# Kernel optimization log

Hardware: AMD Instinct MI355X
Metric: run time of the kernel (lower is better)

The kernel has to match this reference:

```python
import jax, jax.numpy as jnp
import numpy as np

B, F, R, L, P = 16384, 64, 1024, 4, 128  # batch, features, rules, max conditions, interaction pairs


def setup_inputs() -> dict:
    key = jax.random.key(0)
    ks = jax.random.split(key, 8)
    x = jax.random.normal(ks[0], (B, F), dtype=jnp.float32)
    attention_weights = jax.random.uniform(ks[1], (F,), dtype=jnp.float32, minval=0.5, maxval=1.5)
    premise_params = jnp.ones((R,), dtype=jnp.float32)
    rule_threshs = jax.random.normal(ks[2], (R, L), dtype=jnp.float32)
    # signs are +/-1 (split direction of each XGBoost condition)
    rule_signs = jnp.where(jax.random.randint(ks[3], (R, L), 0, 2) == 1, 1.0, -1.0).astype(jnp.float32)
    rule_masks = (jax.random.uniform(ks[4], (R, L)) < 0.9).astype(jnp.float32)
    rule_masks = rule_masks.at[:, 0].set(1.0)
    consequent_params = jax.random.normal(ks[5], (R, 1 + F + F + P), dtype=jnp.float32) * 0.01
    rule_feat_idxs = jax.random.randint(ks[6], (R, L), 0, F)
    interaction_pairs = jax.random.randint(ks[7], (P, 2), 0, F)
    return {
        "x": x,
        "attention_weights": attention_weights,
        "premise_params": premise_params,
        "rule_threshs": rule_threshs,
        "rule_signs": rule_signs,
        "rule_masks": rule_masks,
        "consequent_params": consequent_params,
        "rule_feat_idxs": rule_feat_idxs,
        "interaction_pairs": interaction_pairs,
    }


def reference(x, attention_weights, premise_params, rule_threshs, rule_signs,
              rule_masks, consequent_params, rule_feat_idxs, interaction_pairs):
    # attention scaling
    x_att = x * attention_weights  # [B, F]

    # --- fuzzify_and_infer ---
    sel = x_att[:, rule_feat_idxs]  # gather -> [B, R, L]
    z = premise_params[None, :, None] * (sel - rule_threshs[None]) * rule_signs[None]
    mf = jax.nn.sigmoid(z)
    masked_mf = mf * rule_masks[None] + (1.0 - rule_masks[None])  # inactive conds -> 1
    firing = jnp.prod(masked_mf, axis=2)  # [B, R]
    w = firing / (jnp.sum(firing, axis=1, keepdims=True) + 1e-8)  # normalized firing

    # --- TSK polynomials (order=2 with interactions): [x, x^2, xi*xj, 1] ---
    inter = x_att[:, interaction_pairs[:, 0]] * x_att[:, interaction_pairs[:, 1]]  # [B, P]
    ones = jnp.ones((x.shape[0], 1), dtype=x.dtype)
    p = jnp.concatenate([x_att, x_att * x_att, inter, ones], axis=1)  # [B, 1+2F+P]

    # weighted consequent sum: y_b = sum_r w_br * (p_b . theta_r)
    y = jnp.einsum('br,bi,ri->b', w, p, consequent_params)
    return y
```

## Files before the change

### kernel.cpp

```cpp
#include <hip/hip_runtime.h>

typedef short short8 __attribute__((ext_vector_type(8)));
typedef float f32x4 __attribute__((ext_vector_type(4)));


#define OFF_CP   0ULL
#define OFF_CB   524288ULL
#define OFF_A2   528384ULL
#define OFF_C2   544768ULL
#define OFF_IX   561152ULL
#define OFF_PAIR 565248ULL
#define OFF_NUM  565504ULL
#define OFF_DEN  631040ULL

#define XS 65

__device__ __forceinline__ unsigned short f2bf(float f) {
  unsigned u = __float_as_uint(f);
  return (unsigned short)((u + 0x7FFFu + ((u >> 16) & 1u)) >> 16);
}

__global__ __launch_bounds__(256) void prep_kernel(
    const float* __restrict__ pp, const float* __restrict__ th,
    const float* __restrict__ sg, const float* __restrict__ mk,
    const float* __restrict__ cp, const int* __restrict__ fidx,
    const int* __restrict__ pairs, unsigned char* __restrict__ ws)
{
  unsigned short* cp_out = (unsigned short*)(ws + OFF_CP);
  float* cbo = (float*)(ws + OFF_CB);
  float* a2o = (float*)(ws + OFF_A2);
  float* c2o = (float*)(ws + OFF_C2);
  unsigned* ixo = (unsigned*)(ws + OFF_IX);
  unsigned short* pro = (unsigned short*)(ws + OFF_PAIR);
  int bid = blockIdx.x, t = threadIdx.x;

  if (bid < 256) {
    int e = bid * 1024 + t * 4;
    int r = e >> 8, c = e & 255;
    const float* src = cp + (size_t)r * 257 + c;
#pragma unroll
    for (int q = 0; q < 4; ++q) cp_out[e + q] = f2bf(src[q]);
  } else if (bid < 260) {
    int r = (bid - 256) * 256 + t;
    float p = pp[r];
    unsigned pk = 0;
#pragma unroll
    for (int l = 0; l < 4; ++l) {
      float m = mk[r * 4 + l], s = sg[r * 4 + l], tt = th[r * 4 + l];
      float A, C;
      if (m != 0.f) { A = -1.44269504f * p * s; C = 1.44269504f * p * s * tt; }
      else          { A = 0.f;                  C = -126.f; }
      a2o[r * 4 + l] = A; c2o[r * 4 + l] = C;
      pk |= ((unsigned)fidx[r * 4 + l] & 0xFFu) << (8 * l);
    }
    ixo[r] = pk;
    cbo[r] = cp[(size_t)r * 257 + 256];
  } else if (bid == 260) {
    if (t < 128)
      pro[t] = (unsigned short)((pairs[2 * t] & 0xFF) | ((pairs[2 * t + 1] & 0xFF) << 8));
  } else {
    float* dst = (float*)(ws + (bid == 261 ? OFF_NUM : OFF_DEN));
#pragma unroll
    for (int q = 0; q < 64; ++q) dst[q * 256 + t] = 0.f;
  }
}

__global__ __launch_bounds__(256, 3) void main_kernel(
    const unsigned char* __restrict__ ws,
    const float* __restrict__ x, const float* __restrict__ att,
    float* __restrict__ numg, float* __restrict__ deng)
{
  __shared__ float xa[64 * XS];
  __shared__ short lCP[256 * 32];
  __shared__ short lP[64 * 32];
  __shared__ unsigned short lPair[128];

  const unsigned short* CP = (const unsigned short*)(ws + OFF_CP);
  const float* CB = (const float*)(ws + OFF_CB);
  const float4* A2p = (const float4*)(ws + OFF_A2);
  const float4* C2p = (const float4*)(ws + OFF_C2);
  const unsigned* IX = (const unsigned*)(ws + OFF_IX);
  const unsigned short* PRW = (const unsigned short*)(ws + OFF_PAIR);

  int t = threadIdx.x, l = t & 63, w = t >> 6;
  int g = l >> 4, lr = l & 15;
  int b0 = blockIdx.x * 64, r0 = blockIdx.y * 256;

  if (t < 128) lPair[t] = PRW[t];
  {
#pragma unroll
    for (int i = 0; i < 4; ++i) {
      int idx = t + i * 256, row = idx >> 4, c4 = idx & 15;
      float4 a4 = ((const float4*)att)[c4];
      float4 v = ((const float4*)(x + (size_t)(b0 + row) * 64))[c4];
      float* dst = &xa[row * XS + c4 * 4];
      dst[0] = v.x * a4.x; dst[1] = v.y * a4.y;
      dst[2] = v.z * a4.z; dst[3] = v.w * a4.w;
    }
  }
  __syncthreads();

  f32x4 acc[4][4];
#pragma unroll
  for (int mi = 0; mi < 4; ++mi)
#pragma unroll
    for (int ni = 0; ni < 4; ++ni)
      acc[mi][ni] = (f32x4){0.f, 0.f, 0.f, 0.f};

  int row2 = t >> 2, q = t & 3;
  int sw2 = (row2 ^ (row2 >> 2)) & 3;
  const float* xr2 = &xa[row2 * XS];
  const unsigned short* cpbase = CP + (size_t)(r0 + row2) * 256 + q * 8;

  short8 cpr[2][4];
#pragma unroll
  for (int i = 0; i < 4; ++i) {
    cpr[0][i] = *(const short8*)(cpbase + (size_t)i * 64 * 256);
    cpr[1][i] = *(const short8*)(cpbase + (size_t)i * 64 * 256 + 32);
  }

#pragma unroll 2
  for (int ks = 0; ks < 8; ++ks) {
    int k0 = ks * 32;
    int fb = k0 + q * 8;
    short8 vp;
    if (ks < 2) {
#pragma unroll
      for (int j = 0; j < 8; ++j) vp[j] = f2bf(xr2[fb + j]);
    } else if (ks < 4) {
#pragma unroll
      for (int j = 0; j < 8; ++j) { float u = xr2[fb - 64 + j]; vp[j] = f2bf(u * u); }
    } else {
      const unsigned* pw = (const unsigned*)&lPair[fb - 128];
#pragma unroll
      for (int u = 0; u < 4; ++u) {
        unsigned pk = pw[u];
        vp[2 * u]     = f2bf(xr2[pk & 255] * xr2[(pk >> 8) & 255]);
        vp[2 * u + 1] = f2bf(xr2[(pk >> 16) & 255] * xr2[pk >> 24]);
      }
    }
    __syncthreads();
#pragma unroll
    for (int i = 0; i < 4; ++i) {
      int rowc = row2 + i * 64;
      int swc = (rowc ^ (rowc >> 2)) & 3;
      *(short8*)&lCP[rowc * 32 + ((q ^ swc) * 8)] = cpr[ks & 1][i];
    }
    *(short8*)&lP[row2 * 32 + ((q ^ sw2) * 8)] = vp;
    if (ks < 6) {
#pragma unroll
      for (int i = 0; i < 4; ++i)
        cpr[ks & 1][i] = *(const short8*)(cpbase + (size_t)i * 64 * 256 + k0 + 64);
    }
    __syncthreads();
    short8 bF[4];
#pragma unroll
    for (int ni = 0; ni < 4; ++ni) {
      int row = ni * 16 + lr;
      int s = (row ^ (row >> 2)) & 3;
      bF[ni] = *(const short8*)&lP[row * 32 + ((g ^ s) * 8)];
    }
#pragma unroll
    for (int mi = 0; mi < 4; ++mi) {
      int row = w * 64 + mi * 16 + lr;
      int s = (row ^ (row >> 2)) & 3;
      short8 aF = *(const short8*)&lCP[row * 32 + ((g ^ s) * 8)];
#pragma unroll
      for (int ni = 0; ni < 4; ++ni)
        acc[mi][ni] = __builtin_amdgcn_mfma_f32_16x16x32_bf16(aF, bF[ni], acc[mi][ni], 0, 0, 0);
    }
  }

  float num[4] = {0.f, 0.f, 0.f, 0.f}, den[4] = {0.f, 0.f, 0.f, 0.f};
#pragma unroll
  for (int mi = 0; mi < 4; ++mi) {
#pragma unroll
    for (int j = 0; j < 4; ++j) {
      int rule = r0 + w * 64 + mi * 16 + (g << 2) + j;
      float4 A2 = A2p[rule], C2 = C2p[rule];
      unsigned pk = IX[rule];
      float bias = CB[rule];
      int f0 = pk & 255, f1 = (pk >> 8) & 255, f2 = (pk >> 16) & 255, f3 = pk >> 24;
#pragma unroll
      for (int ni = 0; ni < 4; ++ni) {
        const float* xr = &xa[(ni * 16 + lr) * XS];
        float D = 1.f;
        float e0 = exp2f(fmaf(A2.x, xr[f0], C2.x)); D = fmaf(D, e0, D);
        float e1 = exp2f(fmaf(A2.y, xr[f1], C2.y)); D = fmaf(D, e1, D);
        float e2 = exp2f(fmaf(A2.z, xr[f2], C2.z)); D = fmaf(D, e2, D);
        float e3 = exp2f(fmaf(A2.w, xr[f3], C2.w)); D = fmaf(D, e3, D);
        float fir = __builtin_amdgcn_rcpf(D);
        num[ni] = fmaf(fir, acc[mi][ni][j] + bias, num[ni]);
        den[ni] += fir;
      }
    }
  }

#pragma unroll
  for (int ni = 0; ni < 4; ++ni) {
    float n = num[ni], d = den[ni];
    n += __shfl_xor(n, 16, 64); n += __shfl_xor(n, 32, 64);
    d += __shfl_xor(d, 16, 64); d += __shfl_xor(d, 32, 64);
    num[ni] = n; den[ni] = d;
  }
  float nv = 0.f, dv = 0.f;
#pragma unroll
  for (int ni = 0; ni < 4; ++ni)
    if (g == ni) { nv = num[ni]; dv = den[ni]; }
  atomicAdd(&numg[b0 + (g << 4) + lr], nv);
  atomicAdd(&deng[b0 + (g << 4) + lr], dv);
}

__global__ __launch_bounds__(256) void fin_kernel(
    const float* __restrict__ numg, const float* __restrict__ deng,
    float* __restrict__ y)
{
  int i = blockIdx.x * 256 + threadIdx.x;
  y[i] = numg[i] / (deng[i] + 1e-8f);
}

extern "C" void kernel_launch(void* const* d_in, const int* in_sizes, int n_in,
                              void* d_out, int out_size, void* d_ws, size_t ws_size,
                              hipStream_t stream) {
  (void)in_sizes; (void)n_in; (void)out_size; (void)ws_size;
  const float* x    = (const float*)d_in[0];
  const float* att  = (const float*)d_in[1];
  const float* pp   = (const float*)d_in[2];
  const float* th   = (const float*)d_in[3];
  const float* sg   = (const float*)d_in[4];
  const float* mk   = (const float*)d_in[5];
  const float* cp   = (const float*)d_in[6];
  const int* fidx   = (const int*)d_in[7];
  const int* pairs  = (const int*)d_in[8];
  unsigned char* ws = (unsigned char*)d_ws;
  float* numg = (float*)(ws + OFF_NUM);
  float* deng = (float*)(ws + OFF_DEN);

  prep_kernel<<<263, 256, 0, stream>>>(pp, th, sg, mk, cp, fidx, pairs, ws);
  main_kernel<<<dim3(256, 4), 256, 0, stream>>>(ws, x, att, numg, deng);
  fin_kernel<<<64, 256, 0, stream>>>(numg, deng, (float*)d_out);
}
```

Measured before the change: 107.5 us.

## Precompute bf16 polynomial features in prep kernel and stream MFMA operands from global

The prep kernel now materializes the bf16 polynomial feature matrix P (x, x^2, pair products) for the whole batch in the workspace, so it is built once instead of being recomputed by every rule-tile block. The main kernel drops its LDS staging of CP and P, along with the double-buffered loop and its barriers, and loads MFMA fragments directly from global/L2. It uses 128-rule tiles (8 y-blocks) with a smaller accumulator and targets 4 blocks per CU. The cost is an extra 8 MB workspace round trip and uncoalesced, L2-dependent fragment loads in place of shared-memory reuse.

```diff
diff --git a/kernel.cpp b/kernel.cpp
--- a/kernel.cpp
+++ b/kernel.cpp
@@ -5,13 +5,13 @@
 
 
 #define OFF_CP   0ULL
-#define OFF_CB   524288ULL
-#define OFF_A2   528384ULL
-#define OFF_C2   544768ULL
-#define OFF_IX   561152ULL
-#define OFF_PAIR 565248ULL
-#define OFF_NUM  565504ULL
-#define OFF_DEN  631040ULL
+#define OFF_P    524288ULL
+#define OFF_CB   8912896ULL
+#define OFF_A2   8916992ULL
+#define OFF_C2   8933376ULL
+#define OFF_IX   8949760ULL
+#define OFF_NUM  8953856ULL
+#define OFF_DEN  9019392ULL
 
 #define XS 65
 
@@ -21,27 +21,64 @@
 }
 
 __global__ __launch_bounds__(256) void prep_kernel(
+    const float* __restrict__ x, const float* __restrict__ att,
     const float* __restrict__ pp, const float* __restrict__ th,
     const float* __restrict__ sg, const float* __restrict__ mk,
     const float* __restrict__ cp, const int* __restrict__ fidx,
     const int* __restrict__ pairs, unsigned char* __restrict__ ws)
 {
+  __shared__ float xa[64 * XS];
+  unsigned short* p_out  = (unsigned short*)(ws + OFF_P);
   unsigned short* cp_out = (unsigned short*)(ws + OFF_CP);
   float* cbo = (float*)(ws + OFF_CB);
   float* a2o = (float*)(ws + OFF_A2);
   float* c2o = (float*)(ws + OFF_C2);
   unsigned* ixo = (unsigned*)(ws + OFF_IX);
-  unsigned short* pro = (unsigned short*)(ws + OFF_PAIR);
   int bid = blockIdx.x, t = threadIdx.x;
 
   if (bid < 256) {
-    int e = bid * 1024 + t * 4;
+    int b0 = bid * 64;
+#pragma unroll
+    for (int i = 0; i < 4; ++i) {
+      int idx = t + i * 256, row = idx >> 4, c4 = idx & 15;
+      float4 a4 = ((const float4*)att)[c4];
+      float4 v = ((const float4*)(x + (size_t)(b0 + row) * 64))[c4];
+      float* dst = &xa[row * XS + c4 * 4];
+      dst[0] = v.x * a4.x; dst[1] = v.y * a4.y;
+      dst[2] = v.z * a4.z; dst[3] = v.w * a4.w;
+    }
+    __syncthreads();
+    int row2 = t >> 2, q = t & 3;
+    const float* xr2 = &xa[row2 * XS];
+    unsigned short* po = p_out + (size_t)(b0 + row2) * 256;
+#pragma unroll
+    for (int ks = 0; ks < 8; ++ks) {
+      int fb = ks * 32 + q * 8;
+      short8 vp;
+      if (ks < 2) {
+#pragma unroll
+        for (int j = 0; j < 8; ++j) vp[j] = f2bf(xr2[fb + j]);
+      } else if (ks < 4) {
+#pragma unroll
+        for (int j = 0; j < 8; ++j) { float u = xr2[fb - 64 + j]; vp[j] = f2bf(u * u); }
+      } else {
+        const int2* pr = (const int2*)pairs + (fb - 128);
+#pragma unroll
+        for (int j = 0; j < 8; ++j) {
+          int2 pq = pr[j];
+          vp[j] = f2bf(xr2[pq.x] * xr2[pq.y]);
+        }
+      }
+      *(short8*)(po + fb) = vp;
+    }
+  } else if (bid < 512) {
+    int e = (bid - 256) * 1024 + t * 4;
     int r = e >> 8, c = e & 255;
     const float* src = cp + (size_t)r * 257 + c;
 #pragma unroll
     for (int q = 0; q < 4; ++q) cp_out[e + q] = f2bf(src[q]);
-  } else if (bid < 260) {
-    int r = (bid - 256) * 256 + t;
+  } else if (bid < 516) {
+    int r = (bid - 512) * 256 + t;
     float p = pp[r];
     unsigned pk = 0;
 #pragma unroll
@@ -55,38 +92,31 @@
     }
     ixo[r] = pk;
     cbo[r] = cp[(size_t)r * 257 + 256];
-  } else if (bid == 260) {
-    if (t < 128)
-      pro[t] = (unsigned short)((pairs[2 * t] & 0xFF) | ((pairs[2 * t + 1] & 0xFF) << 8));
   } else {
-    float* dst = (float*)(ws + (bid == 261 ? OFF_NUM : OFF_DEN));
+    float* dst = (float*)(ws + (bid == 516 ? OFF_NUM : OFF_DEN));
 #pragma unroll
     for (int q = 0; q < 64; ++q) dst[q * 256 + t] = 0.f;
   }
 }
 
-__global__ __launch_bounds__(256, 3) void main_kernel(
+__global__ __launch_bounds__(256, 4) void main_kernel(
     const unsigned char* __restrict__ ws,
     const float* __restrict__ x, const float* __restrict__ att,
     float* __restrict__ numg, float* __restrict__ deng)
 {
   __shared__ float xa[64 * XS];
-  __shared__ short lCP[256 * 32];
-  __shared__ short lP[64 * 32];
-  __shared__ unsigned short lPair[128];
 
   const unsigned short* CP = (const unsigned short*)(ws + OFF_CP);
+  const unsigned short* P  = (const unsigned short*)(ws + OFF_P);
   const float* CB = (const float*)(ws + OFF_CB);
   const float4* A2p = (const float4*)(ws + OFF_A2);
   const float4* C2p = (const float4*)(ws + OFF_C2);
   const unsigned* IX = (const unsigned*)(ws + OFF_IX);
-  const unsigned short* PRW = (const unsigned short*)(ws + OFF_PAIR);
 
   int t = threadIdx.x, l = t & 63, w = t >> 6;
   int g = l >> 4, lr = l & 15;
-  int b0 = blockIdx.x * 64, r0 = blockIdx.y * 256;
-
-  if (t < 128) lPair[t] = PRW[t];
+  int b0 = blockIdx.x * 64, r0 = blockIdx.y * 128;
+
   {
 #pragma unroll
     for (int i = 0; i < 4; ++i) {
@@ -100,83 +130,41 @@
   }
   __syncthreads();
 
-  f32x4 acc[4][4];
-#pragma unroll
-  for (int mi = 0; mi < 4; ++mi)
+  const short8* aB0 = (const short8*)(CP + (size_t)(r0 + w * 32 + lr) * 256 + g * 8);
+  const short8* aB1 = (const short8*)(CP + (size_t)(r0 + w * 32 + 16 + lr) * 256 + g * 8);
+  const short8* bB0 = (const short8*)(P + (size_t)(b0 + lr) * 256 + g * 8);
+  const short8* bB1 = (const short8*)(P + (size_t)(b0 + 16 + lr) * 256 + g * 8);
+  const short8* bB2 = (const short8*)(P + (size_t)(b0 + 32 + lr) * 256 + g * 8);
+  const short8* bB3 = (const short8*)(P + (size_t)(b0 + 48 + lr) * 256 + g * 8);
+
+  f32x4 acc[2][4];
+#pragma unroll
+  for (int mi = 0; mi < 2; ++mi)
 #pragma unroll
     for (int ni = 0; ni < 4; ++ni)
       acc[mi][ni] = (f32x4){0.f, 0.f, 0.f, 0.f};
 
-  int row2 = t >> 2, q = t & 3;
-  int sw2 = (row2 ^ (row2 >> 2)) & 3;
-  const float* xr2 = &xa[row2 * XS];
-  const unsigned short* cpbase = CP + (size_t)(r0 + row2) * 256 + q * 8;
-
-  short8 cpr[2][4];
-#pragma unroll
-  for (int i = 0; i < 4; ++i) {
-    cpr[0][i] = *(const short8*)(cpbase + (size_t)i * 64 * 256);
-    cpr[1][i] = *(const short8*)(cpbase + (size_t)i * 64 * 256 + 32);
-  }
-
-#pragma unroll 2
+#pragma unroll
   for (int ks = 0; ks < 8; ++ks) {
-    int k0 = ks * 32;
-    int fb = k0 + q * 8;
-    short8 vp;
-    if (ks < 2) {
-#pragma unroll
-      for (int j = 0; j < 8; ++j) vp[j] = f2bf(xr2[fb + j]);
-    } else if (ks < 4) {
-#pragma unroll
-      for (int j = 0; j < 8; ++j) { float u = xr2[fb - 64 + j]; vp[j] = f2bf(u * u); }
-    } else {
-      const unsigned* pw = (const unsigned*)&lPair[fb - 128];
-#pragma unroll
-      for (int u = 0; u < 4; ++u) {
-        unsigned pk = pw[u];
-        vp[2 * u]     = f2bf(xr2[pk & 255] * xr2[(pk >> 8) & 255]);
-        vp[2 * u + 1] = f2bf(xr2[(pk >> 16) & 255] * xr2[pk >> 24]);
-      }
-    }
-    __syncthreads();
-#pragma unroll
-    for (int i = 0; i < 4; ++i) {
-      int rowc = row2 + i * 64;
-      int swc = (rowc ^ (rowc >> 2)) & 3;
-      *(short8*)&lCP[rowc * 32 + ((q ^ swc) * 8)] = cpr[ks & 1][i];
-    }
-    *(short8*)&lP[row2 * 32 + ((q ^ sw2) * 8)] = vp;
-    if (ks < 6) {
-#pragma unroll
-      for (int i = 0; i < 4; ++i)
-        cpr[ks & 1][i] = *(const short8*)(cpbase + (size_t)i * 64 * 256 + k0 + 64);
-    }
-    __syncthreads();
-    short8 bF[4];
-#pragma unroll
-    for (int ni = 0; ni < 4; ++ni) {
-      int row = ni * 16 + lr;
-      int s = (row ^ (row >> 2)) & 3;
-      bF[ni] = *(const short8*)&lP[row * 32 + ((g ^ s) * 8)];
-    }
-#pragma unroll
-    for (int mi = 0; mi < 4; ++mi) {
-      int row = w * 64 + mi * 16 + lr;
-      int s = (row ^ (row >> 2)) & 3;
-      short8 aF = *(const short8*)&lCP[row * 32 + ((g ^ s) * 8)];
-#pragma unroll
-      for (int ni = 0; ni < 4; ++ni)
-        acc[mi][ni] = __builtin_amdgcn_mfma_f32_16x16x32_bf16(aF, bF[ni], acc[mi][ni], 0, 0, 0);
-    }
+    int ko = ks * 4;
+    short8 a0 = aB0[ko], a1 = aB1[ko];
+    short8 f0 = bB0[ko], f1 = bB1[ko], f2 = bB2[ko], f3 = bB3[ko];
+    acc[0][0] = __builtin_amdgcn_mfma_f32_16x16x32_bf16(a0, f0, acc[0][0], 0, 0, 0);
+    acc[0][1] = __builtin_amdgcn_mfma_f32_16x16x32_bf16(a0, f1, acc[0][1], 0, 0, 0);
+    acc[0][2] = __builtin_amdgcn_mfma_f32_16x16x32_bf16(a0, f2, acc[0][2], 0, 0, 0);
+    acc[0][3] = __builtin_amdgcn_mfma_f32_16x16x32_bf16(a0, f3, acc[0][3], 0, 0, 0);
+    acc[1][0] = __builtin_amdgcn_mfma_f32_16x16x32_bf16(a1, f0, acc[1][0], 0, 0, 0);
+    acc[1][1] = __builtin_amdgcn_mfma_f32_16x16x32_bf16(a1, f1, acc[1][1], 0, 0, 0);
+    acc[1][2] = __builtin_amdgcn_mfma_f32_16x16x32_bf16(a1, f2, acc[1][2], 0, 0, 0);
+    acc[1][3] = __builtin_amdgcn_mfma_f32_16x16x32_bf16(a1, f3, acc[1][3], 0, 0, 0);
   }
 
   float num[4] = {0.f, 0.f, 0.f, 0.f}, den[4] = {0.f, 0.f, 0.f, 0.f};
 #pragma unroll
-  for (int mi = 0; mi < 4; ++mi) {
+  for (int mi = 0; mi < 2; ++mi) {
 #pragma unroll
     for (int j = 0; j < 4; ++j) {
-      int rule = r0 + w * 64 + mi * 16 + (g << 2) + j;
+      int rule = r0 + w * 32 + mi * 16 + (g << 2) + j;
       float4 A2 = A2p[rule], C2 = C2p[rule];
       unsigned pk = IX[rule];
       float bias = CB[rule];
@@ -236,7 +224,7 @@
   float* numg = (float*)(ws + OFF_NUM);
   float* deng = (float*)(ws + OFF_DEN);
 
-  prep_kernel<<<263, 256, 0, stream>>>(pp, th, sg, mk, cp, fidx, pairs, ws);
-  main_kernel<<<dim3(256, 4), 256, 0, stream>>>(ws, x, att, numg, deng);
+  prep_kernel<<<518, 256, 0, stream>>>(x, att, pp, th, sg, mk, cp, fidx, pairs, ws);
+  main_kernel<<<dim3(256, 8), 256, 0, stream>>>(ws, x, att, numg, deng);
   fin_kernel<<<64, 256, 0, stream>>>(numg, deng, (float*)d_out);
 }
```

Measured after the change: 135.4 us. +25.9%, slower.
